# Performance work log

Measured on AMD Instinct MI355X. Metric: run time of the kernel, lower is better.

## Reference

```python
import jax, jax.numpy as jnp
import numpy as np

N = 50000      # node_num
DIN = 128      # input_dim
DH = 128       # hidden_dim
DE = 128       # embedding_dim
DD = 128       # decoder_dim
NE = 800000    # num edges (before self loops)
B = 4096       # drug pairs
EPS = 1e-5


def setup_inputs() -> dict:
    key = jax.random.key(0)
    ks = jax.random.split(key, 16)
    x = jax.random.normal(ks[0], (N, DIN), jnp.float32)
    edge_index = jax.random.randint(ks[1], (2, NE), 0, N, dtype=jnp.int32)
    drug_index = jax.random.randint(ks[2], (B, 2), 0, N, dtype=jnp.int32)
    s = 0.05  # weight scale for numerical sanity
    return {
        "x": x,
        "edge_index": edge_index,
        "drug_index": drug_index,
        "w1": jax.random.normal(ks[3], (DIN, DH), jnp.float32) * s,
        "b1": jnp.zeros((DH,), jnp.float32),
        "w2": jax.random.normal(ks[4], (DH, DH), jnp.float32) * s,
        "b2": jnp.zeros((DH,), jnp.float32),
        "w3": jax.random.normal(ks[5], (DH, DE), jnp.float32) * s,
        "b3": jnp.zeros((DE,), jnp.float32),
        "g1": jnp.ones((DH,), jnp.float32), "be1": jnp.zeros((DH,), jnp.float32),
        "g2": jnp.ones((DH,), jnp.float32), "be2": jnp.zeros((DH,), jnp.float32),
        "g3": jnp.ones((DE,), jnp.float32), "be3": jnp.zeros((DE,), jnp.float32),
        "p1": jax.random.normal(ks[6], (DE, DD), jnp.float32) * s,
        "p2": jax.random.normal(ks[7], (DD, DD), jnp.float32) * s,
    }


def gcn_conv(x, row, col, W, b):
    # row/col already include self loops; PyG: message from row (source), aggregated at col (target)
    n = x.shape[0]
    h = x @ W + b                                   # linear first, as in GCNConv.forward
    deg = jnp.zeros((n,), h.dtype).at[col].add(1.0)  # degree(col) incl. self loops -> >= 1
    dis = deg ** -0.5
    norm = dis[row] * dis[col]                      # [E+N]
    msg = norm[:, None] * h[row]                    # [E+N, d] gather
    return jax.ops.segment_sum(msg, col, num_segments=n)  # scatter-add


def batch_norm(x, gamma, beta):
    m = jnp.mean(x, axis=0)
    v = jnp.mean((x - m) ** 2, axis=0)  # biased var, as torch BatchNorm training
    return (x - m) * jax.lax.rsqrt(v + EPS) * gamma + beta


def leaky(x):
    return jnp.where(x >= 0, x, 0.1 * x)  # LeakyReLU(0.1)


def reference(x, edge_index, drug_index, w1, b1, w2, b2, w3, b3,
              g1, be1, g2, be2, g3, be3, p1, p2):
    n = x.shape[0]
    self_loop = jnp.arange(n, dtype=edge_index.dtype)
    row = jnp.concatenate([edge_index[0], self_loop])
    col = jnp.concatenate([edge_index[1], self_loop])

    h = leaky(batch_norm(gcn_conv(x, row, col, w1, b1), g1, be1))
    h = leaky(batch_norm(gcn_conv(h, row, col, w2, b2), g2, be2))
    h = leaky(batch_norm(gcn_conv(h, row, col, w3, b3), g3, be3))

    di = drug_index.reshape(-1, 2)
    a = h[di[:, 0] - 1]  # [B, DE] (1-based indices; -1 wraps like torch negative index)
    bb = h[di[:, 1] - 1]  # [B, DE]
    t = a @ p1 @ p2 @ p1.T            # [B, DE] bilinear decode, batched
    ypred = jnp.sum(t * bb, axis=1, keepdims=True)  # [B, 1]
    return ypred
```

## Files before the change

### kernel.cpp

```cpp
#include <hip/hip_runtime.h>

#define PAD 64
#define NSLOT 64

__global__ void init_kernel(int* __restrict__ cnt, float* __restrict__ stats, int n, int nstat) {
  int i = blockIdx.x * blockDim.x + threadIdx.x;
  int stride = gridDim.x * blockDim.x;
  for (int j = i; j < n; j += stride) cnt[j] = 0;
  for (int j = i; j < nstat; j += stride) stats[j] = 0.f;
}

__global__ void fillcsr_kernel(const int* __restrict__ row, const int* __restrict__ col,
                               int* __restrict__ cnt, int* __restrict__ csr, int ne) {
  int e = blockIdx.x * blockDim.x + threadIdx.x;
  if (e < ne) {
    int d = col[e];
    int p = atomicAdd(&cnt[d], 1);
    if (p < PAD) csr[d * PAD + p] = row[e];
  }
}

__global__ __launch_bounds__(256, 4) void gemm_kernel(
    const float* __restrict__ A, const float* __restrict__ W, const float* __restrict__ bias,
    float* __restrict__ out, int n, float invN,
    const float* __restrict__ bn_sum, const float* __restrict__ bn_sq,
    const float* __restrict__ bn_g, const float* __restrict__ bn_b, int use_bn,
    const int* __restrict__ cnt) {
  __shared__ float Ws[32 * 128];
  __shared__ float xs[32 * 128];
  __shared__ float bnsc[128], bnsh[128];
  int tid = threadIdx.x;
  if (tid < 128) {
    if (use_bn) {
      float s = 0.f, q = 0.f;
      for (int r2 = 0; r2 < NSLOT; ++r2) { s += bn_sum[r2 * 128 + tid]; q += bn_sq[r2 * 128 + tid]; }
      float m = s * invN;
      float var = q * invN - m * m;
      float rs = rsqrtf(var + 1e-5f);
      float sc = rs * bn_g[tid];
      bnsc[tid] = sc;
      bnsh[tid] = bn_b[tid] - m * sc;
    } else {
      bnsc[tid] = 1.f; bnsh[tid] = 0.f;
    }
  }
  int base = blockIdx.x * 128;
  int tx = tid & 15, ty = tid >> 4;
  int c0 = tx * 4, r0 = ty * 4;
  int r = tid & 127;
  int row_s = base + r;
  int hf = tid >> 7;
  int kw = tid >> 5;
  int c4 = tid & 31;
  const float4* Arow = (const float4*)(A + (size_t)row_s * 128);
  float acc[8][8];
#pragma unroll
  for (int i = 0; i < 8; ++i)
#pragma unroll
    for (int j = 0; j < 8; ++j) acc[i][j] = 0.f;

  for (int kp = 0; kp < 4; ++kp) {
    __syncthreads();
#pragma unroll
    for (int it = 0; it < 4; ++it) {
      int kl = kw + it * 8;
      float4 wv = ((const float4*)(W + (size_t)(kp * 32 + kl) * 128))[c4];
      *(float4*)&Ws[kl * 128 + c4 * 4] = wv;
    }
#pragma unroll
    for (int it = 0; it < 4; ++it) {
      int kbl = hf + it * 2;
      float4 v = make_float4(0.f, 0.f, 0.f, 0.f);
      if (row_s < n) v = Arow[kp * 8 + kbl];
      if (use_bn) {
        int k0 = kp * 32 + kbl * 4;
        float t;
        t = v.x * bnsc[k0 + 0] + bnsh[k0 + 0]; v.x = t >= 0.f ? t : 0.1f * t;
        t = v.y * bnsc[k0 + 1] + bnsh[k0 + 1]; v.y = t >= 0.f ? t : 0.1f * t;
        t = v.z * bnsc[k0 + 2] + bnsh[k0 + 2]; v.z = t >= 0.f ? t : 0.1f * t;
        t = v.w * bnsc[k0 + 3] + bnsh[k0 + 3]; v.w = t >= 0.f ? t : 0.1f * t;
      }
      int kl = kbl * 4;
      xs[(kl + 0) * 128 + r] = v.x;
      xs[(kl + 1) * 128 + r] = v.y;
      xs[(kl + 2) * 128 + r] = v.z;
      xs[(kl + 3) * 128 + r] = v.w;
    }
    __syncthreads();
#pragma unroll 4
    for (int k = 0; k < 32; ++k) {
      float4 a0 = *(const float4*)&xs[k * 128 + r0];
      float4 a1 = *(const float4*)&xs[k * 128 + 64 + r0];
      float4 w0 = *(const float4*)&Ws[k * 128 + c0];
      float4 w1 = *(const float4*)&Ws[k * 128 + 64 + c0];
      float xr[8], wc[8];
      xr[0] = a0.x; xr[1] = a0.y; xr[2] = a0.z; xr[3] = a0.w;
      xr[4] = a1.x; xr[5] = a1.y; xr[6] = a1.z; xr[7] = a1.w;
      wc[0] = w0.x; wc[1] = w0.y; wc[2] = w0.z; wc[3] = w0.w;
      wc[4] = w1.x; wc[5] = w1.y; wc[6] = w1.z; wc[7] = w1.w;
#pragma unroll
      for (int i = 0; i < 8; ++i)
#pragma unroll
        for (int j = 0; j < 8; ++j)
          acc[i][j] = fmaf(xr[i], wc[j], acc[i][j]);
    }
  }
  float bb0[4], bb1[4];
#pragma unroll
  for (int j = 0; j < 4; ++j) { bb0[j] = bias[c0 + j]; bb1[j] = bias[64 + c0 + j]; }
#pragma unroll
  for (int i = 0; i < 8; ++i) {
    int row = base + (i < 4 ? r0 + i : 64 + r0 + (i - 4));
    if (row < n) {
      float rs = rsqrtf((float)(cnt[row] + 1));
      float4 o0, o1;
      o0.x = (acc[i][0] + bb0[0]) * rs; o0.y = (acc[i][1] + bb0[1]) * rs;
      o0.z = (acc[i][2] + bb0[2]) * rs; o0.w = (acc[i][3] + bb0[3]) * rs;
      o1.x = (acc[i][4] + bb1[0]) * rs; o1.y = (acc[i][5] + bb1[1]) * rs;
      o1.z = (acc[i][6] + bb1[2]) * rs; o1.w = (acc[i][7] + bb1[3]) * rs;
      *(float4*)&out[(size_t)row * 128 + c0] = o0;
      *(float4*)&out[(size_t)row * 128 + 64 + c0] = o1;
    }
  }
}

__global__ __launch_bounds__(256) void agg_kernel(const float* __restrict__ z,
                                                  const int* __restrict__ cnt,
                                                  const int* __restrict__ csr,
                                                  float* __restrict__ out,
                                                  float* __restrict__ Ssum,
                                                  float* __restrict__ Ssq,
                                                  int n, int half) {
  __shared__ float bs[4][128], bq[4][128];
  int tid = threadIdx.x;
  int lane = tid & 63;
  int wv = tid >> 6;
  int w = (blockIdx.x * blockDim.x + tid) >> 6;
  float stx = 0.f, sty = 0.f, qtx = 0.f, qty = 0.f;
  if (w < half) {
    int i0 = w, i1 = w + half;
    bool has1 = (i1 < n);
    const float2* __restrict__ h2 = (const float2*)z;
    unsigned off0 = (unsigned)i0 * 64u + (unsigned)lane;
    unsigned off1 = (unsigned)i1 * 64u + (unsigned)lane;
    float2 self0 = h2[off0];
    float2 self1 = has1 ? h2[off1] : make_float2(0.f, 0.f);
    int c0r = cnt[i0];
    int c1r = has1 ? cnt[i1] : 0;
    float d0 = rsqrtf((float)(c0r + 1));
    float d1 = rsqrtf((float)(c1r + 1));
    int e0 = c0r > PAD ? PAD : c0r;
    int e1 = c1r > PAD ? PAD : c1r;
    const int* __restrict__ lp0 = csr + (size_t)i0 * PAD;
    const int* __restrict__ lp1 = csr + (size_t)i1 * PAD;
    float s0x = self0.x, s0y = self0.y;
    float s1x = self1.x, s1y = self1.y;
    int my0 = (lane < e0) ? lp0[lane] : 0;
    int my1 = (lane < e1) ? lp1[lane] : 0;
    int p0 = 0, p1 = 0;
    while (p0 + 8 <= e0 && p1 + 8 <= e1) {
      float2 v0[8], v1[8];
#pragma unroll
      for (int u = 0; u < 8; ++u) { int s = __shfl(my0, p0 + u, 64); v0[u] = h2[(unsigned)s * 64u + (unsigned)lane]; }
#pragma unroll
      for (int u = 0; u < 8; ++u) { int s = __shfl(my1, p1 + u, 64); v1[u] = h2[(unsigned)s * 64u + (unsigned)lane]; }
#pragma unroll
      for (int u = 0; u < 8; ++u) {
        s0x += v0[u].x; s0y += v0[u].y;
        s1x += v1[u].x; s1y += v1[u].y;
      }
      p0 += 8; p1 += 8;
    }
    for (; p0 + 8 <= e0; p0 += 8) {
      float2 v[8];
#pragma unroll
      for (int u = 0; u < 8; ++u) { int s = __shfl(my0, p0 + u, 64); v[u] = h2[(unsigned)s * 64u + (unsigned)lane]; }
#pragma unroll
      for (int u = 0; u < 8; ++u) { s0x += v[u].x; s0y += v[u].y; }
    }
    for (; p0 + 4 <= e0; p0 += 4) {
      float2 v[4];
#pragma unroll
      for (int u = 0; u < 4; ++u) { int s = __shfl(my0, p0 + u, 64); v[u] = h2[(unsigned)s * 64u + (unsigned)lane]; }
#pragma unroll
      for (int u = 0; u < 4; ++u) { s0x += v[u].x; s0y += v[u].y; }
    }
    for (; p0 < e0; ++p0) {
      int s = __shfl(my0, p0, 64);
      float2 v = h2[(unsigned)s * 64u + (unsigned)lane];
      s0x += v.x; s0y += v.y;
    }
    for (; p1 + 8 <= e1; p1 += 8) {
      float2 v[8];
#pragma unroll
      for (int u = 0; u < 8; ++u) { int s = __shfl(my1, p1 + u, 64); v[u] = h2[(unsigned)s * 64u + (unsigned)lane]; }
#pragma unroll
      for (int u = 0; u < 8; ++u) { s1x += v[u].x; s1y += v[u].y; }
    }
    for (; p1 + 4 <= e1; p1 += 4) {
      float2 v[4];
#pragma unroll
      for (int u = 0; u < 4; ++u) { int s = __shfl(my1, p1 + u, 64); v[u] = h2[(unsigned)s * 64u + (unsigned)lane]; }
#pragma unroll
      for (int u = 0; u < 4; ++u) { s1x += v[u].x; s1y += v[u].y; }
    }
    for (; p1 < e1; ++p1) {
      int s = __shfl(my1, p1, 64);
      float2 v = h2[(unsigned)s * 64u + (unsigned)lane];
      s1x += v.x; s1y += v.y;
    }
    float2 o0; o0.x = d0 * s0x; o0.y = d0 * s0y;
    ((float2*)out)[off0] = o0;
    stx += o0.x; qtx = fmaf(o0.x, o0.x, qtx);
    sty += o0.y; qty = fmaf(o0.y, o0.y, qty);
    if (has1) {
      float2 o1; o1.x = d1 * s1x; o1.y = d1 * s1y;
      ((float2*)out)[off1] = o1;
      stx += o1.x; qtx = fmaf(o1.x, o1.x, qtx);
      sty += o1.y; qty = fmaf(o1.y, o1.y, qty);
    }
  }
  bs[wv][2 * lane] = stx;     bs[wv][2 * lane + 1] = sty;
  bq[wv][2 * lane] = qtx;     bq[wv][2 * lane + 1] = qty;
  __syncthreads();
  if (tid < 128) {
    float s = bs[0][tid] + bs[1][tid] + bs[2][tid] + bs[3][tid];
    float q = bq[0][tid] + bq[1][tid] + bq[2][tid] + bq[3][tid];
    int slot = (blockIdx.x & (NSLOT - 1)) * 128 + tid;
    atomicAdd(&Ssum[slot], s);
    atomicAdd(&Ssq[slot], q);
  }
}

__global__ __launch_bounds__(128) void mm128_kernel(const float* __restrict__ A, const float* __restrict__ B,
                                                    float* __restrict__ C, int transB) {
  __shared__ float Ar[128];
  int i = blockIdx.x, j = threadIdx.x;
  Ar[j] = A[i * 128 + j];
  __syncthreads();
  float acc = 0.f;
  if (transB) {
    for (int k = 0; k < 128; ++k) acc = fmaf(Ar[k], B[j * 128 + k], acc);
  } else {
    for (int k = 0; k < 128; ++k) acc = fmaf(Ar[k], B[k * 128 + j], acc);
  }
  C[i * 128 + j] = acc;
}

__global__ __launch_bounds__(256) void decoder_kernel(
    const float* __restrict__ h, const int* __restrict__ di, const float* __restrict__ M,
    const float* __restrict__ bn_sum, const float* __restrict__ bn_sq,
    const float* __restrict__ bn_g, const float* __restrict__ bn_b,
    float* __restrict__ out, int npairs, int n, float invN) {
  __shared__ float Ms[128 * 128];
  __shared__ float sc[128], sh[128];
  int tid = threadIdx.x;
  if (tid < 128) {
    float s = 0.f, q = 0.f;
    for (int r2 = 0; r2 < NSLOT; ++r2) { s += bn_sum[r2 * 128 + tid]; q += bn_sq[r2 * 128 + tid]; }
    float m = s * invN;
    float var = q * invN - m * m;
    float rs = rsqrtf(var + 1e-5f);
    float scv = rs * bn_g[tid];
    sc[tid] = scv;
    sh[tid] = bn_b[tid] - m * scv;
  }
  for (int t = tid; t < 4096; t += 256) ((float4*)Ms)[t] = ((const float4*)M)[t];
  __syncthreads();
  int lane = tid & 63, wv = tid >> 6;
  int wid = blockIdx.x * 4 + wv;
  int nw = gridDim.x * 4;
  for (int k = wid; k < npairs; k += nw) {
    int ia = di[2 * k] - 1;     if (ia < 0) ia += n;
    int ib = di[2 * k + 1] - 1; if (ib < 0) ib += n;
    const float* ap = h + (size_t)ia * 128;
    const float* bp = h + (size_t)ib * 128;
    float u0 = 0.f, u1 = 0.f;
#pragma unroll 8
    for (int i = 0; i < 128; ++i) {
      float av = ap[i] * sc[i] + sh[i];
      av = av >= 0.f ? av : 0.1f * av;
      u0 = fmaf(av, Ms[i * 128 + lane], u0);
      u1 = fmaf(av, Ms[i * 128 + 64 + lane], u1);
    }
    float b0 = bp[lane] * sc[lane] + sh[lane];            b0 = b0 >= 0.f ? b0 : 0.1f * b0;
    float b1 = bp[lane + 64] * sc[lane + 64] + sh[lane + 64]; b1 = b1 >= 0.f ? b1 : 0.1f * b1;
    float part = u0 * b0 + u1 * b1;
#pragma unroll
    for (int o = 32; o; o >>= 1) part += __shfl_down(part, o, 64);
    if (lane == 0) out[k] = part;
  }
}

extern "C" void kernel_launch(void* const* d_in, const int* in_sizes, int n_in,
                              void* d_out, int out_size, void* d_ws, size_t ws_size,
                              hipStream_t stream) {
  const float* x   = (const float*)d_in[0];
  const int*   ei  = (const int*)d_in[1];
  const int*   dri = (const int*)d_in[2];
  const float* w1  = (const float*)d_in[3];
  const float* b1  = (const float*)d_in[4];
  const float* w2  = (const float*)d_in[5];
  const float* b2  = (const float*)d_in[6];
  const float* w3  = (const float*)d_in[7];
  const float* b3  = (const float*)d_in[8];
  const float* g1  = (const float*)d_in[9];
  const float* be1 = (const float*)d_in[10];
  const float* g2  = (const float*)d_in[11];
  const float* be2 = (const float*)d_in[12];
  const float* g3  = (const float*)d_in[13];
  const float* be3 = (const float*)d_in[14];
  const float* p1  = (const float*)d_in[15];
  const float* p2  = (const float*)d_in[16];
  float* out = (float*)d_out;

  int n  = in_sizes[0] / 128;
  int ne = in_sizes[1] / 2;
  int np = in_sizes[2] / 2;
  const int* erow = ei;
  const int* ecol = ei + ne;

  size_t o = 0;
  char* wsb = (char*)d_ws;
  auto alloc = [&](size_t bytes) { void* p = wsb + o; o += (bytes + 255) & ~255ull; return p; };
  float* T1   = (float*)alloc((size_t)n * 128 * 4);
  float* T2   = (float*)alloc((size_t)n * 128 * 4);
  int*   csr  = (int*)alloc((size_t)n * PAD * 4);
  int*   cnt  = (int*)alloc((size_t)n * 4);
  int nstat = 6 * NSLOT * 128;
  float* stats = (float*)alloc((size_t)nstat * 4);
  float* M1   = (float*)alloc(128 * 128 * 4);
  float* M2   = (float*)alloc(128 * 128 * 4);
  float* Ssum1 = stats;
  float* Ssq1  = stats + 1 * NSLOT * 128;
  float* Ssum2 = stats + 2 * NSLOT * 128;
  float* Ssq2  = stats + 3 * NSLOT * 128;
  float* Ssum3 = stats + 4 * NSLOT * 128;
  float* Ssq3  = stats + 5 * NSLOT * 128;

  float invN = 1.0f / (float)n;
  int eb = (ne + 255) / 256;
  int gb = (n + 127) / 128;
  int half = (n + 1) / 2;
  int ab = (half + 3) / 4;

  init_kernel<<<512, 256, 0, stream>>>(cnt, stats, n, nstat);
  fillcsr_kernel<<<eb, 256, 0, stream>>>(erow, ecol, cnt, csr, ne);

  gemm_kernel<<<gb, 256, 0, stream>>>(x, w1, b1, T1, n, invN, nullptr, nullptr, nullptr, nullptr, 0, cnt);
  agg_kernel<<<ab, 256, 0, stream>>>(T1, cnt, csr, T2, Ssum1, Ssq1, n, half);

  gemm_kernel<<<gb, 256, 0, stream>>>(T2, w2, b2, T1, n, invN, Ssum1, Ssq1, g1, be1, 1, cnt);
  agg_kernel<<<ab, 256, 0, stream>>>(T1, cnt, csr, T2, Ssum2, Ssq2, n, half);

  gemm_kernel<<<gb, 256, 0, stream>>>(T2, w3, b3, T1, n, invN, Ssum2, Ssq2, g2, be2, 1, cnt);
  agg_kernel<<<ab, 256, 0, stream>>>(T1, cnt, csr, T2, Ssum3, Ssq3, n, half);

  mm128_kernel<<<128, 128, 0, stream>>>(p1, p2, M1, 0);
  mm128_kernel<<<128, 128, 0, stream>>>(M1, p1, M2, 1);
  decoder_kernel<<<256, 256, 0, stream>>>(T2, dri, M2, Ssum3, Ssq3, g3, be3, out, np, n, invN);
}
```

Baseline: 383.4 us.

## Fuse decoder weight product into init kernel and shuffle-broadcast decoder row

The two small 128x128 matrix-product kernels that build p1·p2·p1ᵀ are removed. That product is now computed by one extra block appended to the init kernel, which removes two launches and a dependent serial step. The init kernel also runs 256 zeroing blocks instead of 512. In the decoder, each lane loads a float2 of the left drug row and normalizes it once, then broadcasts values with wavefront shuffles, so the 128 scalar global loads per pair are gone. The risk is that a single block must finish the 128x128x128 chain inside the init kernel, which could lengthen that kernel's tail.

```diff
diff --git a/kernel.cpp b/kernel.cpp
--- a/kernel.cpp
+++ b/kernel.cpp
@@ -3,11 +3,43 @@
 #define PAD 64
 #define NSLOT 64
 
-__global__ void init_kernel(int* __restrict__ cnt, float* __restrict__ stats, int n, int nstat) {
-  int i = blockIdx.x * blockDim.x + threadIdx.x;
-  int stride = gridDim.x * blockDim.x;
-  for (int j = i; j < n; j += stride) cnt[j] = 0;
-  for (int j = i; j < nstat; j += stride) stats[j] = 0.f;
+__global__ __launch_bounds__(256) void init_kernel(int* __restrict__ cnt, float* __restrict__ stats,
+                                                   int n, int nstat,
+                                                   const float* __restrict__ p1,
+                                                   const float* __restrict__ p2,
+                                                   float* __restrict__ M2) {
+  if (blockIdx.x < 256) {
+    int i = blockIdx.x * 256 + threadIdx.x;
+    int stride = 256 * 256;
+    for (int j = i; j < n; j += stride) cnt[j] = 0;
+    for (int j = i; j < nstat; j += stride) stats[j] = 0.f;
+    return;
+  }
+  __shared__ float Mtmp[128 * 128];
+  __shared__ float prow[2 * 128];
+  int tid = threadIdx.x;
+  int jj = tid & 127;
+  int ii = tid >> 7;
+  for (int ip = 0; ip < 64; ++ip) {
+    __syncthreads();
+    prow[tid] = p1[(2 * ip + ii) * 128 + jj];
+    __syncthreads();
+    float acc = 0.f;
+    const float* pr = &prow[ii * 128];
+#pragma unroll 4
+    for (int k = 0; k < 128; ++k) acc = fmaf(pr[k], p2[k * 128 + jj], acc);
+    Mtmp[(2 * ip + ii) * 128 + jj] = acc;
+  }
+  __syncthreads();
+  for (int ip = 0; ip < 64; ++ip) {
+    int i = 2 * ip + ii;
+    const float* mr = &Mtmp[i * 128];
+    const float* pj = p1 + (size_t)jj * 128;
+    float acc = 0.f;
+#pragma unroll 4
+    for (int l = 0; l < 128; ++l) acc = fmaf(mr[l], pj[l], acc);
+    M2[i * 128 + jj] = acc;
+  }
 }
 
 __global__ void fillcsr_kernel(const int* __restrict__ row, const int* __restrict__ col,
@@ -232,21 +264,6 @@
   }
 }
 
-__global__ __launch_bounds__(128) void mm128_kernel(const float* __restrict__ A, const float* __restrict__ B,
-                                                    float* __restrict__ C, int transB) {
-  __shared__ float Ar[128];
-  int i = blockIdx.x, j = threadIdx.x;
-  Ar[j] = A[i * 128 + j];
-  __syncthreads();
-  float acc = 0.f;
-  if (transB) {
-    for (int k = 0; k < 128; ++k) acc = fmaf(Ar[k], B[j * 128 + k], acc);
-  } else {
-    for (int k = 0; k < 128; ++k) acc = fmaf(Ar[k], B[k * 128 + j], acc);
-  }
-  C[i * 128 + j] = acc;
-}
-
 __global__ __launch_bounds__(256) void decoder_kernel(
     const float* __restrict__ h, const int* __restrict__ di, const float* __restrict__ M,
     const float* __restrict__ bn_sum, const float* __restrict__ bn_sq,
@@ -273,17 +290,23 @@
   for (int k = wid; k < npairs; k += nw) {
     int ia = di[2 * k] - 1;     if (ia < 0) ia += n;
     int ib = di[2 * k + 1] - 1; if (ib < 0) ib += n;
-    const float* ap = h + (size_t)ia * 128;
+    const float2* ap2 = (const float2*)(h + (size_t)ia * 128);
     const float* bp = h + (size_t)ib * 128;
+    float2 a2 = ap2[lane];
+    float ax = a2.x * sc[2 * lane] + sh[2 * lane];         ax = ax >= 0.f ? ax : 0.1f * ax;
+    float ay = a2.y * sc[2 * lane + 1] + sh[2 * lane + 1]; ay = ay >= 0.f ? ay : 0.1f * ay;
     float u0 = 0.f, u1 = 0.f;
 #pragma unroll 8
-    for (int i = 0; i < 128; ++i) {
-      float av = ap[i] * sc[i] + sh[i];
-      av = av >= 0.f ? av : 0.1f * av;
-      u0 = fmaf(av, Ms[i * 128 + lane], u0);
-      u1 = fmaf(av, Ms[i * 128 + 64 + lane], u1);
-    }
-    float b0 = bp[lane] * sc[lane] + sh[lane];            b0 = b0 >= 0.f ? b0 : 0.1f * b0;
+    for (int i2 = 0; i2 < 64; ++i2) {
+      float avx = __shfl(ax, i2, 64);
+      float avy = __shfl(ay, i2, 64);
+      int i = 2 * i2;
+      u0 = fmaf(avx, Ms[i * 128 + lane], u0);
+      u1 = fmaf(avx, Ms[i * 128 + 64 + lane], u1);
+      u0 = fmaf(avy, Ms[(i + 1) * 128 + lane], u0);
+      u1 = fmaf(avy, Ms[(i + 1) * 128 + 64 + lane], u1);
+    }
+    float b0 = bp[lane] * sc[lane] + sh[lane];                b0 = b0 >= 0.f ? b0 : 0.1f * b0;
     float b1 = bp[lane + 64] * sc[lane + 64] + sh[lane + 64]; b1 = b1 >= 0.f ? b1 : 0.1f * b1;
     float part = u0 * b0 + u1 * b1;
 #pragma unroll
@@ -329,7 +352,6 @@
   int*   cnt  = (int*)alloc((size_t)n * 4);
   int nstat = 6 * NSLOT * 128;
   float* stats = (float*)alloc((size_t)nstat * 4);
-  float* M1   = (float*)alloc(128 * 128 * 4);
   float* M2   = (float*)alloc(128 * 128 * 4);
   float* Ssum1 = stats;
   float* Ssq1  = stats + 1 * NSLOT * 128;
@@ -344,7 +366,7 @@
   int half = (n + 1) / 2;
   int ab = (half + 3) / 4;
 
-  init_kernel<<<512, 256, 0, stream>>>(cnt, stats, n, nstat);
+  init_kernel<<<257, 256, 0, stream>>>(cnt, stats, n, nstat, p1, p2, M2);
   fillcsr_kernel<<<eb, 256, 0, stream>>>(erow, ecol, cnt, csr, ne);
 
   gemm_kernel<<<gb, 256, 0, stream>>>(x, w1, b1, T1, n, invN, nullptr, nullptr, nullptr, nullptr, 0, cnt);
@@ -356,7 +378,5 @@
   gemm_kernel<<<gb, 256, 0, stream>>>(T2, w3, b3, T1, n, invN, Ssum2, Ssq2, g2, be2, 1, cnt);
   agg_kernel<<<ab, 256, 0, stream>>>(T1, cnt, csr, T2, Ssum3, Ssq3, n, half);
 
-  mm128_kernel<<<128, 128, 0, stream>>>(p1, p2, M1, 0);
-  mm128_kernel<<<128, 128, 0, stream>>>(M1, p1, M2, 1);
   decoder_kernel<<<256, 256, 0, stream>>>(T2, dri, M2, Ssum3, Ssq3, g3, be3, out, np, n, invN);
 }
```

Measured after the change: 830.4 us. 2.17x slower.
